# Performance work log

Hardware: AMD Instinct MI355X
Metric: run time of the kernel (lower is better)

The kernel has to match this reference:

```python
import jax, jax.numpy as jnp
import numpy as np

D = 131072  # inner feature dim
N = 84      # 4*(1 + 4*(1 + 4)) entries emitted by calc_probs


def calc_probs(logits):
    # softmax over the 4 logits, then emit, in original nested-loop order:
    # for i: p_i, then for j: p_i*p_j followed by p_i*p_j*p_k for k in 0..3
    p = jax.nn.softmax(logits)                      # (4,)
    pairs = p[:, None] * p[None, :]                 # (4,4)
    triples = pairs[:, :, None] * p[None, None, :]  # (4,4,4)
    inner = jnp.concatenate([pairs[:, :, None], triples], axis=2)  # (4,4,5)
    full = jnp.concatenate([p[:, None], inner.reshape(4, 20)], axis=1)  # (4,21)
    return full.reshape(N)  # (84,)


def setup_inputs() -> dict:
    key = jax.random.key(0)
    ks = jax.random.split(key, 6)
    return {
        "BEV": jax.random.normal(ks[0], (1,), dtype=jnp.float32),
        "ST0": jax.random.normal(ks[1], (N, D), dtype=jnp.float32),
        "Weight0": jax.random.normal(ks[2], (N, D, 1), dtype=jnp.float32),
        "ST1": jax.random.normal(ks[3], (N, D), dtype=jnp.float32),
        "Weight1": jax.random.normal(ks[4], (N, D, 1), dtype=jnp.float32),
        "Problem": 1,
        "probs0": jnp.array([2.0327, 1.0198, 1.024, 0.9935], dtype=jnp.float32),
        "probs1": jnp.array([2.6661, 1.0168, 1.02, 0.9971], dtype=jnp.float32),
        "probs2": jnp.array([2.8173, 1.016, 1.0189, 0.9978], dtype=jnp.float32),
        "probs3": jnp.array([2.9183, 1.0154, 1.0181, 0.9981], dtype=jnp.float32),
        "probs4": jnp.array([2.9689, 1.0151, 1.0177, 0.9983], dtype=jnp.float32),
        "pBEV": jnp.array([0.1822], dtype=jnp.float32),
        "pB": jnp.array([3.1475], dtype=jnp.float32),
    }


def reference(BEV, ST0, Weight0, ST1, Weight1, Problem,
              probs0, probs1, probs2, probs3, probs4, pBEV, pB):
    p0 = calc_probs(probs0)
    p1 = calc_probs(probs1)
    p2 = calc_probs(probs2)
    p3 = calc_probs(probs3)
    p4 = calc_probs(probs4)
    # fused sigmoid + per-row dot, replacing the Python loop over 84 rows
    bev = pBEV * BEV  # (1,)
    tmp0 = jnp.einsum('id,id->i', jax.nn.sigmoid(pB * (bev + ST0)), Weight0[..., 0])  # (84,)
    tmp1 = jnp.einsum('id,id->i', jax.nn.sigmoid(pB * (bev + ST1)), Weight1[..., 0])  # (84,)
    vals = jnp.stack([p0 @ tmp0, p1 @ tmp1, p2 @ tmp1, p3 @ tmp1, p4 @ tmp1])
    return jnp.mean(vals)
```

## Files before the change

### kernel.cpp

```cpp
#include <hip/hip_runtime.h>


#define D_DIM          131072
#define N_ROWS         84
#define ROW_F4         (D_DIM / 4)
#define F4_PER_CHUNK   1024
#define CHUNK_BYTES    (F4_PER_CHUNK * 16)
#define CPB            4
#define BLOCKS_PER_ROW (ROW_F4 / (F4_PER_CHUNK * CPB))
#define T0_BLOCKS      (N_ROWS * BLOCKS_PER_ROW)
#define BLOCKS         (2 * T0_BLOCKS)

typedef float f32x4 __attribute__((ext_vector_type(4)));

__device__ inline float prob_entry(const float* __restrict__ logits, int t) {
    float l0 = logits[0], l1 = logits[1], l2 = logits[2], l3 = logits[3];
    float m  = fmaxf(fmaxf(l0, l1), fmaxf(l2, l3));
    float e0 = __expf(l0 - m), e1 = __expf(l1 - m);
    float e2 = __expf(l2 - m), e3 = __expf(l3 - m);
    float inv = 1.0f / (e0 + e1 + e2 + e3);
    float p[4] = {e0 * inv, e1 * inv, e2 * inv, e3 * inv};
    int i = t / 21;
    int r = t - i * 21;
    if (r == 0) return p[i];
    r -= 1;
    int j = r / 5;
    int s = r - j * 5;
    float v = p[i] * p[j];
    return (s == 0) ? v : v * p[s - 1];
}

__device__ inline float sigdot(float w, float s, float a, float ab) {
    float e = __builtin_amdgcn_exp2f(fmaf(a, s, ab));
    return w * __builtin_amdgcn_rcpf(1.0f + e);
}

#define ISSUE8(S0, S1, S2, S3, Wa, Wb_, Wc, Wd, off, SB, WB)               \
    asm volatile(                                                          \
        "global_load_dwordx4 %0, %8, %12\n\t"                              \
        "global_load_dwordx4 %4, %8, %13\n\t"                              \
        "global_load_dwordx4 %1, %9, %12\n\t"                              \
        "global_load_dwordx4 %5, %9, %13\n\t"                              \
        "global_load_dwordx4 %2, %10, %12\n\t"                             \
        "global_load_dwordx4 %6, %10, %13\n\t"                             \
        "global_load_dwordx4 %3, %11, %12\n\t"                             \
        "global_load_dwordx4 %7, %11, %13"                                 \
        : "=&v"(S0), "=&v"(S1), "=&v"(S2), "=&v"(S3),                      \
          "=&v"(Wa), "=&v"(Wb_), "=&v"(Wc), "=&v"(Wd)                      \
        : "v"(off), "v"((off) + 4096u), "v"((off) + 8192u),                \
          "v"((off) + 12288u), "s"(SB), "s"(WB))

#define WAIT_PREV8(S0, S1, S2, S3, Wa, Wb_, Wc, Wd)                        \
    asm volatile("s_waitcnt vmcnt(8)"                                      \
                 : "+v"(S0), "+v"(S1), "+v"(S2), "+v"(S3),                 \
                   "+v"(Wa), "+v"(Wb_), "+v"(Wc), "+v"(Wd))

#define WAIT_ALL8(S0, S1, S2, S3, Wa, Wb_, Wc, Wd)                         \
    asm volatile("s_waitcnt vmcnt(0)"                                      \
                 : "+v"(S0), "+v"(S1), "+v"(S2), "+v"(S3),                 \
                   "+v"(Wa), "+v"(Wb_), "+v"(Wc), "+v"(Wd))

#define ACC16(S0, S1, S2, S3, Wa, Wb_, Wc, Wd)                             \
    do {                                                                   \
        acc += sigdot(Wa[0], S0[0], a, ab);                                \
        acc += sigdot(Wa[1], S0[1], a, ab);                                \
        acc += sigdot(Wa[2], S0[2], a, ab);                                \
        acc += sigdot(Wa[3], S0[3], a, ab);                                \
        acc += sigdot(Wb_[0], S1[0], a, ab);                               \
        acc += sigdot(Wb_[1], S1[1], a, ab);                               \
        acc += sigdot(Wb_[2], S1[2], a, ab);                               \
        acc += sigdot(Wb_[3], S1[3], a, ab);                               \
        acc += sigdot(Wc[0], S2[0], a, ab);                                \
        acc += sigdot(Wc[1], S2[1], a, ab);                                \
        acc += sigdot(Wc[2], S2[2], a, ab);                                \
        acc += sigdot(Wc[3], S2[3], a, ab);                                \
        acc += sigdot(Wd[0], S3[0], a, ab);                                \
        acc += sigdot(Wd[1], S3[1], a, ab);                                \
        acc += sigdot(Wd[2], S3[2], a, ab);                                \
        acc += sigdot(Wd[3], S3[3], a, ab);                                \
    } while (0)

__global__ __launch_bounds__(256, 4) void probsnet_main(
    const float* __restrict__ BEV,
    const float* __restrict__ ST0, const float* __restrict__ W0,
    const float* __restrict__ ST1, const float* __restrict__ W1,
    const float* __restrict__ probs0, const float* __restrict__ probs1,
    const float* __restrict__ probs2, const float* __restrict__ probs3,
    const float* __restrict__ probs4,
    const float* __restrict__ pBEV, const float* __restrict__ pB,
    float* __restrict__ partials)
{
    const int bid    = blockIdx.x;
    const int t      = threadIdx.x;
    const int tensor = (bid >= T0_BLOCKS) ? 1 : 0;
    const int cb     = bid - tensor * T0_BLOCKS;
    const int row    = cb / BLOCKS_PER_ROW;

    const float pb  = pB[0];
    const float bev = pBEV[0] * BEV[0];
    const float a   = -pb * 1.4426950408889634f;
    const float ab  = a * bev;

    const float* Sb = tensor ? ST1 : ST0;
    const float* Wb = tensor ? W1  : W0;

    const unsigned base = (unsigned)(cb * (CPB * F4_PER_CHUNK) + t) * 16u;

    f32x4 as0, as1, as2, as3, aw0, aw1, aw2, aw3;
    f32x4 bs0, bs1, bs2, bs3, bw0, bw1, bw2, bw3;

    float acc = 0.0f;

    ISSUE8(as0, as1, as2, as3, aw0, aw1, aw2, aw3, base,                   Sb, Wb);
    ISSUE8(bs0, bs1, bs2, bs3, bw0, bw1, bw2, bw3, base + 1u * CHUNK_BYTES, Sb, Wb);

    WAIT_PREV8(as0, as1, as2, as3, aw0, aw1, aw2, aw3);
    ACC16(as0, as1, as2, as3, aw0, aw1, aw2, aw3);
    ISSUE8(as0, as1, as2, as3, aw0, aw1, aw2, aw3, base + 2u * CHUNK_BYTES, Sb, Wb);

    WAIT_PREV8(bs0, bs1, bs2, bs3, bw0, bw1, bw2, bw3);
    ACC16(bs0, bs1, bs2, bs3, bw0, bw1, bw2, bw3);
    ISSUE8(bs0, bs1, bs2, bs3, bw0, bw1, bw2, bw3, base + 3u * CHUNK_BYTES, Sb, Wb);

    WAIT_PREV8(as0, as1, as2, as3, aw0, aw1, aw2, aw3);
    ACC16(as0, as1, as2, as3, aw0, aw1, aw2, aw3);

    WAIT_ALL8(bs0, bs1, bs2, bs3, bw0, bw1, bw2, bw3);
    ACC16(bs0, bs1, bs2, bs3, bw0, bw1, bw2, bw3);

    #pragma unroll
    for (int off = 32; off > 0; off >>= 1)
        acc += __shfl_down(acc, off, 64);

    __shared__ float red[4];
    const int wave = t >> 6;
    const int lane = t & 63;
    if (lane == 0) red[wave] = acc;
    __syncthreads();

    if (t == 0) {
        const float S = red[0] + red[1] + red[2] + red[3];
        float pw;
        if (tensor == 0) {
            pw = prob_entry(probs0, row);
        } else {
            pw = prob_entry(probs1, row) + prob_entry(probs2, row)
               + prob_entry(probs3, row) + prob_entry(probs4, row);
        }
        partials[bid] = pw * S;
    }
}

__global__ __launch_bounds__(256) void probsnet_reduce(
    const float* __restrict__ partials, float* __restrict__ out)
{
    const int t = threadIdx.x;
    float acc = 0.0f;
    for (int k = t; k < BLOCKS; k += 256)
        acc += partials[k];

    #pragma unroll
    for (int off = 32; off > 0; off >>= 1)
        acc += __shfl_down(acc, off, 64);

    __shared__ float red[4];
    const int wave = t >> 6;
    const int lane = t & 63;
    if (lane == 0) red[wave] = acc;
    __syncthreads();

    if (t == 0)
        out[0] = (red[0] + red[1] + red[2] + red[3]) * 0.2f;
}

extern "C" void kernel_launch(void* const* d_in, const int* in_sizes, int n_in,
                              void* d_out, int out_size, void* d_ws, size_t ws_size,
                              hipStream_t stream) {
    const float* BEV    = (const float*)d_in[0];
    const float* ST0    = (const float*)d_in[1];
    const float* W0     = (const float*)d_in[2];
    const float* ST1    = (const float*)d_in[3];
    const float* W1     = (const float*)d_in[4];
    const float* probs0 = (const float*)d_in[6];
    const float* probs1 = (const float*)d_in[7];
    const float* probs2 = (const float*)d_in[8];
    const float* probs3 = (const float*)d_in[9];
    const float* probs4 = (const float*)d_in[10];
    const float* pBEV   = (const float*)d_in[11];
    const float* pB     = (const float*)d_in[12];

    float* partials = (float*)d_ws;
    float* out      = (float*)d_out;

    probsnet_main<<<BLOCKS, 256, 0, stream>>>(
        BEV, ST0, W0, ST1, W1,
        probs0, probs1, probs2, probs3, probs4,
        pBEV, pB, partials);

    probsnet_reduce<<<1, 256, 0, stream>>>(partials, out);
}
```

Baseline: 203.7 us.

## Halve per-block work to two chunks and use non-temporal streaming loads

Each block now handles 2048 float4s (two chunks) instead of four, which doubles the grid and removes the in-block double-buffer reissue loop. All global loads gain the nt (non-temporal) cache hint, since the data is streamed once. The intent is more blocks in flight to hide latency and less cache pollution, at the cost of more block launch and reduction overhead and more partials to sum.

```diff
diff --git a/kernel.cpp b/kernel.cpp
--- a/kernel.cpp
+++ b/kernel.cpp
@@ -1,15 +1,13 @@
 #include <hip/hip_runtime.h>
 
 
-#define D_DIM          131072
-#define N_ROWS         84
-#define ROW_F4         (D_DIM / 4)
-#define F4_PER_CHUNK   1024
-#define CHUNK_BYTES    (F4_PER_CHUNK * 16)
-#define CPB            4
-#define BLOCKS_PER_ROW (ROW_F4 / (F4_PER_CHUNK * CPB))
-#define T0_BLOCKS      (N_ROWS * BLOCKS_PER_ROW)
-#define BLOCKS         (2 * T0_BLOCKS)
+#define D_DIM         131072
+#define N_ROWS        84
+#define ROW_F4        (D_DIM / 4)
+#define TENSOR_F4     (N_ROWS * ROW_F4)
+#define F4_PER_BLOCK  2048
+#define T0_BLOCKS     (TENSOR_F4 / F4_PER_BLOCK)
+#define BLOCKS        (2 * T0_BLOCKS)
 
 typedef float f32x4 __attribute__((ext_vector_type(4)));
 
@@ -35,30 +33,26 @@
     return w * __builtin_amdgcn_rcpf(1.0f + e);
 }
 
-#define ISSUE8(S0, S1, S2, S3, Wa, Wb_, Wc, Wd, off, SB, WB)               \
+#define ISSUE8(S0, S1, S2, S3, Wa, Wb_, Wc, Wd, OFFC)                      \
     asm volatile(                                                          \
-        "global_load_dwordx4 %0, %8, %12\n\t"                              \
-        "global_load_dwordx4 %4, %8, %13\n\t"                              \
-        "global_load_dwordx4 %1, %9, %12\n\t"                              \
-        "global_load_dwordx4 %5, %9, %13\n\t"                              \
-        "global_load_dwordx4 %2, %10, %12\n\t"                             \
-        "global_load_dwordx4 %6, %10, %13\n\t"                             \
-        "global_load_dwordx4 %3, %11, %12\n\t"                             \
-        "global_load_dwordx4 %7, %11, %13"                                 \
+        "global_load_dwordx4 %0, %8, %12 nt\n\t"                           \
+        "global_load_dwordx4 %4, %8, %13 nt\n\t"                           \
+        "global_load_dwordx4 %1, %9, %12 nt\n\t"                           \
+        "global_load_dwordx4 %5, %9, %13 nt\n\t"                           \
+        "global_load_dwordx4 %2, %10, %12 nt\n\t"                          \
+        "global_load_dwordx4 %6, %10, %13 nt\n\t"                          \
+        "global_load_dwordx4 %3, %11, %12 nt\n\t"                          \
+        "global_load_dwordx4 %7, %11, %13 nt"                              \
         : "=&v"(S0), "=&v"(S1), "=&v"(S2), "=&v"(S3),                      \
           "=&v"(Wa), "=&v"(Wb_), "=&v"(Wc), "=&v"(Wd)                      \
-        : "v"(off), "v"((off) + 4096u), "v"((off) + 8192u),                \
-          "v"((off) + 12288u), "s"(SB), "s"(WB))
+        : "v"(vbase + (OFFC) + 0u),    "v"(vbase + (OFFC) + 4096u),        \
+          "v"(vbase + (OFFC) + 8192u), "v"(vbase + (OFFC) + 12288u),       \
+          "s"(Sb), "s"(Wb))
 
-#define WAIT_PREV8(S0, S1, S2, S3, Wa, Wb_, Wc, Wd)                        \
-    asm volatile("s_waitcnt vmcnt(8)"                                      \
+#define WAITP(N, S0, S1, S2, S3, Wa, Wb_, Wc, Wd)                          \
+    asm volatile("s_waitcnt vmcnt(%8)"                                     \
                  : "+v"(S0), "+v"(S1), "+v"(S2), "+v"(S3),                 \
-                   "+v"(Wa), "+v"(Wb_), "+v"(Wc), "+v"(Wd))
-
-#define WAIT_ALL8(S0, S1, S2, S3, Wa, Wb_, Wc, Wd)                         \
-    asm volatile("s_waitcnt vmcnt(0)"                                      \
-                 : "+v"(S0), "+v"(S1), "+v"(S2), "+v"(S3),                 \
-                   "+v"(Wa), "+v"(Wb_), "+v"(Wc), "+v"(Wd))
+                   "+v"(Wa), "+v"(Wb_), "+v"(Wc), "+v"(Wd) : "n"(N))
 
 #define ACC16(S0, S1, S2, S3, Wa, Wb_, Wc, Wd)                             \
     do {                                                                   \
@@ -93,8 +87,8 @@
     const int bid    = blockIdx.x;
     const int t      = threadIdx.x;
     const int tensor = (bid >= T0_BLOCKS) ? 1 : 0;
-    const int cb     = bid - tensor * T0_BLOCKS;
-    const int row    = cb / BLOCKS_PER_ROW;
+    const int fb     = (bid - tensor * T0_BLOCKS) * F4_PER_BLOCK;
+    const int row    = fb >> 15;
 
     const float pb  = pB[0];
     const float bev = pBEV[0] * BEV[0];
@@ -104,28 +98,20 @@
     const float* Sb = tensor ? ST1 : ST0;
     const float* Wb = tensor ? W1  : W0;
 
-    const unsigned base = (unsigned)(cb * (CPB * F4_PER_CHUNK) + t) * 16u;
+    const unsigned vbase = (unsigned)(fb + t) * 16u;
 
     f32x4 as0, as1, as2, as3, aw0, aw1, aw2, aw3;
     f32x4 bs0, bs1, bs2, bs3, bw0, bw1, bw2, bw3;
 
+    ISSUE8(as0, as1, as2, as3, aw0, aw1, aw2, aw3, 0u);
+    ISSUE8(bs0, bs1, bs2, bs3, bw0, bw1, bw2, bw3, 16384u);
+
     float acc = 0.0f;
 
-    ISSUE8(as0, as1, as2, as3, aw0, aw1, aw2, aw3, base,                   Sb, Wb);
-    ISSUE8(bs0, bs1, bs2, bs3, bw0, bw1, bw2, bw3, base + 1u * CHUNK_BYTES, Sb, Wb);
-
-    WAIT_PREV8(as0, as1, as2, as3, aw0, aw1, aw2, aw3);
-    ACC16(as0, as1, as2, as3, aw0, aw1, aw2, aw3);
-    ISSUE8(as0, as1, as2, as3, aw0, aw1, aw2, aw3, base + 2u * CHUNK_BYTES, Sb, Wb);
-
-    WAIT_PREV8(bs0, bs1, bs2, bs3, bw0, bw1, bw2, bw3);
-    ACC16(bs0, bs1, bs2, bs3, bw0, bw1, bw2, bw3);
-    ISSUE8(bs0, bs1, bs2, bs3, bw0, bw1, bw2, bw3, base + 3u * CHUNK_BYTES, Sb, Wb);
-
-    WAIT_PREV8(as0, as1, as2, as3, aw0, aw1, aw2, aw3);
+    WAITP(8, as0, as1, as2, as3, aw0, aw1, aw2, aw3);
     ACC16(as0, as1, as2, as3, aw0, aw1, aw2, aw3);
 
-    WAIT_ALL8(bs0, bs1, bs2, bs3, bw0, bw1, bw2, bw3);
+    WAITP(0, bs0, bs1, bs2, bs3, bw0, bw1, bw2, bw3);
     ACC16(bs0, bs1, bs2, bs3, bw0, bw1, bw2, bw3);
 
     #pragma unroll
```

New measurement: 187.1 us. -8.2%, faster.
